# Kernel tuning notes

Hardware: AMD Instinct MI355X
Metric: run time of the kernel (lower is better)

The kernel has to match this reference:

```python
import jax, jax.numpy as jnp
import numpy as np

N, E, B = 25000, 400000, 64      # nodes, edges, graphs per batched graph
NF, EF = 64, 16                  # node / edge input feature sizes
EMB, H = 128, 4                  # GAT embedding size, attention heads
NEG_ATTN, NEG_ACT = 0.2, 0.01    # leaky-relu slopes (attn logits / activations)


def setup_inputs() -> dict:
    keys = iter(jax.random.split(jax.random.key(0), 64))
    def rn(shape, s=0.05):
        return jax.random.normal(next(keys), shape, jnp.float32) * s
    def ri():
        return jax.random.randint(next(keys), (E,), 0, N, jnp.int32)
    # sorted graph ids; construction guarantees every graph is non-empty
    gid = ((jnp.arange(N, dtype=jnp.int32) * B) // N).astype(jnp.int32)
    return dict(
        srcA=ri(), dstA=ri(), gidA=gid,
        nfA=rn((N, NF), 1.0), efA=rn((E, EF), 1.0),
        srcB=ri(), dstB=ri(), gidB=gid,
        nfB=rn((N, NF), 1.0), efB=rn((E, EF), 1.0),
        # stacked params: leading dim 2 = branch (0=A, 1=B)
        p_Wn=rn((2, NF, NF)), p_bn=rn((2, NF)),
        p_We=rn((2, EF, EF)), p_be=rn((2, EF)),
        p_Wc=rn((2, NF + EF, NF + EF)), p_bc=rn((2, NF + EF)),
        p_fc1=rn((2, NF + EF, H * EMB)), p_al1=rn((2, H, EMB)), p_ar1=rn((2, H, EMB)), p_gb1=rn((2, H * EMB)),
        p_Wl1=rn((2, H * EMB, EMB)), p_bl1=rn((2, EMB)),
        p_fc2=rn((2, EMB, H * EMB)), p_al2=rn((2, H, EMB)), p_ar2=rn((2, H, EMB)), p_gb2=rn((2, H * EMB)),
        p_Wl2=rn((2, H * EMB, EMB)), p_bl2=rn((2, EMB)),
        p_ws_w=rn((2, EMB, 1)), p_ws_b=rn((2, 1)),
        p_Wp=rn((2, 2 * EMB, EMB)), p_bp=rn((2, EMB)),
        Wo1=rn((2 * EMB, EMB)), bo1=rn((EMB,)),
        Wo2=rn((EMB, 1)), bo2=rn((1,)),
    )


def _gat(h, src, dst, Wfc, al, ar, bias):
    """DGL GATConv: fc -> per-head attn logits -> edge softmax over dst -> scatter-sum."""
    n = h.shape[0]
    z = (h @ Wfc).reshape(n, al.shape[0], al.shape[1])    # [N,H,D]
    el = jnp.sum(z * al, -1)                              # [N,H]
    er = jnp.sum(z * ar, -1)
    e = jax.nn.leaky_relu(el[src] + er[dst], NEG_ATTN)    # [E,H]
    m = jax.ops.segment_max(e, dst, num_segments=n)
    ex = jnp.exp(e - m[dst])
    a = ex / jax.ops.segment_sum(ex, dst, num_segments=n)[dst]
    rst = jax.ops.segment_sum(a[:, :, None] * z[src], dst, num_segments=n)  # [N,H,D]
    rst = rst + bias.reshape(1, al.shape[0], al.shape[1])
    return jax.nn.leaky_relu(rst, NEG_ACT)                # activation=nn.LeakyReLU()


def _branch(i, src, dst, gid, nf, ef, p):
    n = nf.shape[0]
    # InputInitializer: project nodes/edges, concat src-node feats with edge feats
    hn = nf @ p['p_Wn'][i] + p['p_bn'][i]
    he = ef @ p['p_We'][i] + p['p_be'][i]
    x = jnp.concatenate([hn[src], he], axis=1)            # [E, NF+EF]
    # EdgeGraphConv (in_feats == out_feats -> else-branch): scatter-sum then linear+relu
    x = jax.ops.segment_sum(x, dst, num_segments=n)
    x = jax.nn.relu(x @ p['p_Wc'][i] + p['p_bc'][i])
    # GAT 1 + flatten linear
    x = _gat(x, src, dst, p['p_fc1'][i], p['p_al1'][i], p['p_ar1'][i], p['p_gb1'][i])
    x = x.reshape(n, -1) @ p['p_Wl1'][i] + p['p_bl1'][i]
    # GAT 2 + flatten linear
    x = _gat(x, src, dst, p['p_fc2'][i], p['p_al2'][i], p['p_ar2'][i], p['p_gb2'][i])
    x = x.reshape(n, -1) @ p['p_Wl2'][i] + p['p_bl2'][i]
    # WeightedSumAndMax readout
    w = jax.nn.sigmoid(x @ p['p_ws_w'][i] + p['p_ws_b'][i])
    hs = jax.ops.segment_sum(x * w, gid, num_segments=B)
    hm = jax.ops.segment_max(x, gid, num_segments=B)
    hg = jnp.concatenate([hs, hm], axis=1)                # [B, 2*EMB]
    return hg @ p['p_Wp'][i] + p['p_bp'][i]               # pool_linear


def reference(srcA, dstA, gidA, nfA, efA, srcB, dstB, gidB, nfB, efB,
              p_Wn, p_bn, p_We, p_be, p_Wc, p_bc,
              p_fc1, p_al1, p_ar1, p_gb1, p_Wl1, p_bl1,
              p_fc2, p_al2, p_ar2, p_gb2, p_Wl2, p_bl2,
              p_ws_w, p_ws_b, p_Wp, p_bp, Wo1, bo1, Wo2, bo2):
    p = dict(p_Wn=p_Wn, p_bn=p_bn, p_We=p_We, p_be=p_be, p_Wc=p_Wc, p_bc=p_bc,
             p_fc1=p_fc1, p_al1=p_al1, p_ar1=p_ar1, p_gb1=p_gb1, p_Wl1=p_Wl1, p_bl1=p_bl1,
             p_fc2=p_fc2, p_al2=p_al2, p_ar2=p_ar2, p_gb2=p_gb2, p_Wl2=p_Wl2, p_bl2=p_bl2,
             p_ws_w=p_ws_w, p_ws_b=p_ws_b, p_Wp=p_Wp, p_bp=p_bp)
    x = _branch(0, srcA, dstA, gidA, nfA, efA, p)
    y = _branch(1, srcB, dstB, gidB, nfB, efB, p)
    z = jnp.concatenate([x, y], axis=1)                   # [B, 2*EMB]
    z = jax.nn.leaky_relu(z @ Wo1 + bo1, NEG_ACT)
    return z @ Wo2 + bo2                                  # [B, 1]
```

## Files before the change

### kernel.cpp

```cpp
#include <hip/hip_runtime.h>
#include <hip/hip_bf16.h>
#include <hip/hip_fp16.h>

typedef __hip_bfloat16 bf16;
typedef unsigned short u16;
typedef __attribute__((ext_vector_type(8))) short short8;
typedef __attribute__((ext_vector_type(4))) float floatx4;
typedef _Float16 half8 __attribute__((ext_vector_type(8)));

static constexpr int Nn = 25000;
static constexpr int Ne = 400000;
static constexpr int Bg = 64;

__device__ __forceinline__ float ldf(const void* p, size_t i, bool b16) {
  return b16 ? __bfloat162float(((const bf16*)p)[i]) : ((const float*)p)[i];
}

__global__ void detect_kernel(const u16* a, int n, const u16* b, int m, int* flags) {
  __shared__ int c0, c1;
  if (threadIdx.x == 0) { c0 = 0; c1 = 0; }
  __syncthreads();
  int t = threadIdx.x;
  int l0 = 0, l1 = 0;
  for (int i = t; i < n; i += 256) {
    unsigned e = (a[i] >> 7) & 0xFF;
    if (e >= 140) l0++;
  }
  for (int i = t; i < m; i += 256) {
    unsigned e = (b[i] >> 7) & 0xFF;
    if (e >= 140) l1++;
  }
  atomicAdd(&c0, l0);
  atomicAdd(&c1, l1);
  __syncthreads();
  if (t == 0) {
    flags[0] = (c0 < n / 16) ? 1 : 0;
    flags[1] = (c1 < m / 16) ? 1 : 0;
  }
}

struct TC { const void* W; size_t off; __half* H; int K; int N; int start; };
struct TCAll { TC t[10]; int total; };

__global__ void transconv_all_kernel(TCAll a, const int* __restrict__ pflag) {
  const bool pb = (*pflag != 0);
  int idx = blockIdx.x * 256 + threadIdx.x;
  if (idx >= a.total) return;
  int s = 0;
  while (s + 1 < 10 && idx >= a.t[s + 1].start) s++;
  int li = idx - a.t[s].start;
  int K = a.t[s].K, N = a.t[s].N;
  int k = li / N, n = li - k * N;
  float w = ldf(a.t[s].W, a.t[s].off + li, pb);
  a.t[s].H[(size_t)n * K + k] = __float2half(w);
}

template <int ACT, int OUT>
__global__ __launch_bounds__(256) void mfma_f16_gemm(const __half* __restrict__ A,
                                                     const __half* __restrict__ Bt,
                                                     const void* __restrict__ bias, size_t boff,
                                                     const int* __restrict__ pflag,
                                                     void* __restrict__ C,
                                                     int M, int K, int N) {
  __shared__ short As[128 * 40];
  __shared__ short Bs[128 * 40];
  const int bm = blockIdx.x * 128;
  const int bn = blockIdx.y * 128;
  const int tid = threadIdx.x;
  const int lane = tid & 63;
  const int wave = tid >> 6;
  const int wm = wave >> 1, wn = wave & 1;
  const int lm = lane & 15, quad = lane >> 4;
  const int srow = tid >> 1;
  const int sseg = tid & 1;
  floatx4 acc[4][4] = {};
  for (int k0 = 0; k0 < K; k0 += 32) {
    bool kv = (k0 + sseg * 16) < K;
    {
      int gr = bm + srow;
      short8 a0 = {}, a1 = {};
      if (gr < M && kv) {
        const short8* gp = (const short8*)(A + (size_t)gr * K + k0 + sseg * 16);
        a0 = gp[0];
        a1 = gp[1];
      }
      *(short8*)&As[srow * 40 + sseg * 16] = a0;
      *(short8*)&As[srow * 40 + sseg * 16 + 8] = a1;
    }
    {
      int gc = bn + srow;
      short8 b0 = {}, b1 = {};
      if (gc < N && kv) {
        const short8* gp = (const short8*)(Bt + (size_t)gc * K + k0 + sseg * 16);
        b0 = gp[0];
        b1 = gp[1];
      }
      *(short8*)&Bs[srow * 40 + sseg * 16] = b0;
      *(short8*)&Bs[srow * 40 + sseg * 16 + 8] = b1;
    }
    __syncthreads();
    half8 af[4], bfv[4];
#pragma unroll
    for (int f = 0; f < 4; f++) {
      af[f] = *(const half8*)&As[(wm * 64 + f * 16 + lm) * 40 + quad * 8];
      bfv[f] = *(const half8*)&Bs[(wn * 64 + f * 16 + lm) * 40 + quad * 8];
    }
#pragma unroll
    for (int i = 0; i < 4; i++)
#pragma unroll
      for (int j = 0; j < 4; j++)
        acc[i][j] = __builtin_amdgcn_mfma_f32_16x16x32_f16(af[i], bfv[j], acc[i][j], 0, 0, 0);
    __syncthreads();
  }
  const bool pb = (*pflag != 0);
#pragma unroll
  for (int i = 0; i < 4; i++) {
#pragma unroll
    for (int j = 0; j < 4; j++) {
      int col = bn + wn * 64 + j * 16 + lm;
      if (col >= N) continue;
#pragma unroll
      for (int r = 0; r < 4; r++) {
        int row = bm + wm * 64 + i * 16 + quad * 4 + r;
        if (row >= M) continue;
        float v = acc[i][j][r];
        if (bias) v += ldf(bias, boff + col, pb);
        if (ACT == 1) v = v > 0.f ? v : 0.f;
        if (OUT == 0)
          ((float*)C)[(size_t)row * N + col] = v;
        else
          ((__half*)C)[(size_t)row * N + col] = __float2half(v);
      }
    }
  }
}

__global__ __launch_bounds__(256) void proj_nf_kernel(const void* __restrict__ nfA,
                                                      const void* __restrict__ nfB,
                                                      const int* __restrict__ fflag,
                                                      const void* __restrict__ Wn,
                                                      const void* __restrict__ bn,
                                                      const int* __restrict__ pflag,
                                                      __half* __restrict__ hn, int N) {
  __shared__ float Ws[64 * 65];
  __shared__ float bs[64];
  __shared__ float rowbuf[4][64];
  const bool fb = (*fflag != 0), pb = (*pflag != 0);
  const int b = blockIdx.y;
  const void* nf = b ? nfB : nfA;
  size_t woff = (size_t)b * 64 * 64, boff = (size_t)b * 64;
  int t = threadIdx.x;
  for (int i = t; i < 4096; i += 256) {
    int k = i >> 6, c = i & 63;
    Ws[k * 65 + c] = ldf(Wn, woff + i, pb);
  }
  if (t < 64) bs[t] = ldf(bn, boff + t, pb);
  __syncthreads();
  int wave = t >> 6, lane = t & 63;
  int n = blockIdx.x * 4 + wave;
  if (n >= N) return;
  rowbuf[wave][lane] = ldf(nf, (size_t)n * 64 + lane, fb);
  float acc = bs[lane];
#pragma unroll 8
  for (int k = 0; k < 64; k++) acc += rowbuf[wave][k] * Ws[k * 65 + lane];
  hn[(size_t)b * N * 64 + (size_t)n * 64 + lane] = __float2half(acc);
}

__global__ __launch_bounds__(256) void proj_ef_kernel(const void* __restrict__ efA,
                                                      const void* __restrict__ efB,
                                                      const int* __restrict__ fflag,
                                                      const void* __restrict__ We,
                                                      const void* __restrict__ be,
                                                      const int* __restrict__ pflag,
                                                      __half* __restrict__ he, int E) {
  __shared__ float Ws[16 * 17];
  __shared__ float bs[16];
  __shared__ float efs[16][17];
  const bool fb = (*fflag != 0), pb = (*pflag != 0);
  const int b = blockIdx.y;
  const void* ef = b ? efB : efA;
  size_t woff = (size_t)b * 256, boff = (size_t)b * 16;
  int t = threadIdx.x;
  Ws[(t >> 4) * 17 + (t & 15)] = ldf(We, woff + t, pb);
  if (t < 16) bs[t] = ldf(be, boff + t, pb);
  int el = t >> 4, k = t & 15;
  int e = blockIdx.x * 16 + el;
  float v = 0.f;
  if (e < E) v = ldf(ef, (size_t)e * 16 + k, fb);
  efs[el][k] = v;
  __syncthreads();
  if (e < E) {
    float acc = bs[k];
#pragma unroll
    for (int kk = 0; kk < 16; kk++) acc += efs[el][kk] * Ws[kk * 17 + k];
    he[(size_t)b * E * 16 + (size_t)e * 16 + k] = __float2half(acc);
  }
}

__global__ void count_kernel(const int* __restrict__ dA, const int* __restrict__ dB,
                             int* __restrict__ cnt, int E, int N) {
  int b = blockIdx.y;
  const int* dst = b ? dB : dA;
  int e = blockIdx.x * 256 + threadIdx.x;
  if (e < E) atomicAdd(&cnt[b * N + dst[e]], 1);
}

__global__ void scan1_kernel(const int* __restrict__ cnt, int* __restrict__ incl,
                             int* __restrict__ bsum, int n) {
  __shared__ int buf[256];
  int b = blockIdx.y;
  int t = threadIdx.x;
  int i = blockIdx.x * 256 + t;
  int v = (i < n) ? cnt[b * n + i] : 0;
  buf[t] = v;
  __syncthreads();
  for (int d = 1; d < 256; d <<= 1) {
    int add = (t >= d) ? buf[t - d] : 0;
    __syncthreads();
    buf[t] += add;
    __syncthreads();
  }
  if (i < n) incl[b * n + i] = buf[t];
  if (t == 255) bsum[b * 256 + blockIdx.x] = buf[255];
}

__global__ void scan2_kernel(int* __restrict__ bsum, int nb) {
  __shared__ int buf[256];
  int b = blockIdx.x;
  int t = threadIdx.x;
  int v = (t < nb) ? bsum[b * 256 + t] : 0;
  buf[t] = v;
  __syncthreads();
  for (int d = 1; d < 256; d <<= 1) {
    int add = (t >= d) ? buf[t - d] : 0;
    __syncthreads();
    buf[t] += add;
    __syncthreads();
  }
  if (t < nb) bsum[b * 256 + t] = buf[t] - v;
}

__global__ void scan3_kernel(const int* __restrict__ cnt, const int* __restrict__ incl,
                             const int* __restrict__ bsum, int* __restrict__ offs,
                             int* __restrict__ cursor, int n) {
  int b = blockIdx.y;
  int i = blockIdx.x * 256 + threadIdx.x;
  if (i < n) {
    int e = incl[b * n + i] - cnt[b * n + i] + bsum[b * 256 + blockIdx.x];
    offs[b * (n + 1) + i] = e;
    cursor[b * n + i] = e;
    if (i == n - 1) offs[b * (n + 1) + n] = incl[b * n + i] + bsum[b * 256 + blockIdx.x];
  }
}

__global__ void fill_kernel(const int* __restrict__ dA, const int* __restrict__ dB,
                            int* __restrict__ cursor, int* __restrict__ perm, int E, int N) {
  int b = blockIdx.y;
  const int* dst = b ? dB : dA;
  int e = blockIdx.x * 256 + threadIdx.x;
  if (e < E) {
    int p = atomicAdd(&cursor[b * N + dst[e]], 1);
    perm[(size_t)b * E + p] = e;
  }
}

__global__ __launch_bounds__(64) void sortseg_kernel(const int* __restrict__ off,
                                                     int* __restrict__ perm, int N, int E) {
  __shared__ int loc[64 * 64];
  int b = blockIdx.y;
  const int* offb = off + b * (N + 1);
  int* permb = perm + (size_t)b * E;
  int t = threadIdx.x;
  int n = blockIdx.x * 64 + t;
  if (n >= N) return;
  int e0 = offb[n], e1 = offb[n + 1];
  int d = e1 - e0;
  if (d <= 1) return;
  if (d <= 64) {
    for (int i = 0; i < d; i++) loc[i * 64 + t] = permb[e0 + i];
    for (int i = 1; i < d; i++) {
      int v = loc[i * 64 + t];
      int j = i - 1;
      while (j >= 0 && loc[j * 64 + t] > v) { loc[(j + 1) * 64 + t] = loc[j * 64 + t]; j--; }
      loc[(j + 1) * 64 + t] = v;
    }
    for (int i = 0; i < d; i++) permb[e0 + i] = loc[i * 64 + t];
  } else {
    for (int i = 0; i < d - 1; i++) {
      int mi = i;
      for (int j = i + 1; j < d; j++)
        if (permb[e0 + j] < permb[e0 + mi]) mi = j;
      int tmp = permb[e0 + i];
      permb[e0 + i] = permb[e0 + mi];
      permb[e0 + mi] = tmp;
    }
  }
}

__global__ void srccsr_kernel(const int* __restrict__ sA, const int* __restrict__ sB,
                              const int* __restrict__ perm, int* __restrict__ src_csr, int E) {
  int b = blockIdx.y;
  const int* src = b ? sB : sA;
  int i = blockIdx.x * 256 + threadIdx.x;
  if (i < E) src_csr[(size_t)b * E + i] = src[perm[(size_t)b * E + i]];
}

__global__ __launch_bounds__(128) void edgeconv_kernel(const int* __restrict__ off,
                                                       const int* __restrict__ perm,
                                                       const int* __restrict__ src_csr,
                                                       const __half* __restrict__ hn,
                                                       const __half* __restrict__ he,
                                                       __half* __restrict__ xsum, int N, int E) {
  int b = blockIdx.y;
  const int* offb = off + b * (N + 1);
  const int* permb = perm + (size_t)b * E;
  const int* scb = src_csr + (size_t)b * E;
  const __half* hnb = hn + (size_t)b * N * 64;
  const __half* heb = he + (size_t)b * E * 16;
  int n = blockIdx.x;
  int f = threadIdx.x;
  if (n >= N || f >= 80) return;
  int e0 = offb[n], e1 = offb[n + 1];
  float acc = 0.f;
  if (f < 64) {
    int eg = e0;
    for (; eg + 4 <= e1; eg += 4) {
      int s0 = scb[eg], s1 = scb[eg + 1], s2 = scb[eg + 2], s3 = scb[eg + 3];
      float v0 = __half2float(hnb[(size_t)s0 * 64 + f]);
      float v1 = __half2float(hnb[(size_t)s1 * 64 + f]);
      float v2 = __half2float(hnb[(size_t)s2 * 64 + f]);
      float v3 = __half2float(hnb[(size_t)s3 * 64 + f]);
      acc += v0; acc += v1; acc += v2; acc += v3;
    }
    for (; eg < e1; eg++) acc += __half2float(hnb[(size_t)scb[eg] * 64 + f]);
  } else {
    int c = f - 64;
    for (int eg = e0; eg < e1; eg++) acc += __half2float(heb[(size_t)permb[eg] * 16 + c]);
  }
  xsum[(size_t)b * N * 80 + (size_t)n * 80 + f] = __float2half(acc);
}

__global__ __launch_bounds__(256) void attn_lr_kernel(const __half* __restrict__ z,
                                                      const void* __restrict__ al,
                                                      const void* __restrict__ ar, size_t off,
                                                      const int* __restrict__ pflag,
                                                      float* __restrict__ el,
                                                      float* __restrict__ er, int N) {
  const bool pb = (*pflag != 0);
  int n = (blockIdx.x * blockDim.x + threadIdx.x) >> 6;
  int lane = threadIdx.x & 63;
  if (n >= N) return;
  union { uint4 q; __half s[8]; } u;
  u.q = *(const uint4*)(z + (size_t)n * 512 + lane * 8);
  float sl = 0.f, sr = 0.f;
#pragma unroll
  for (int q = 0; q < 8; q++) {
    int idx = lane * 8 + q;
    float zv = __half2float(u.s[q]);
    sl += zv * ldf(al, off + idx, pb);
    sr += zv * ldf(ar, off + idx, pb);
  }
#pragma unroll
  for (int o = 1; o < 16; o <<= 1) {
    sl += __shfl_xor(sl, o);
    sr += __shfl_xor(sr, o);
  }
  if ((lane & 15) == 0) {
    int h = lane >> 4;
    el[n * 4 + h] = sl;
    er[n * 4 + h] = sr;
  }
}

__global__ void attn_sden_kernel(const int* __restrict__ off, const int* __restrict__ src_csr,
                                 const float* __restrict__ el, const float* __restrict__ er,
                                 float* __restrict__ ecsr, float* __restrict__ sden, int N) {
  int idx = blockIdx.x * 256 + threadIdx.x;
  int n = idx >> 2, h = idx & 3;
  if (n >= N) return;
  int e0 = off[n], e1 = off[n + 1];
  float ern = er[n * 4 + h];
  float s = 0.f;
  for (int eg = e0; eg < e1; eg++) {
    float v = el[src_csr[eg] * 4 + h] + ern;
    v = v > 0.f ? v : 0.2f * v;
    v = fminf(v, 60.f);
    float ev = expf(v);
    ecsr[eg * 4 + h] = ev;
    s += ev;
  }
  sden[n * 4 + h] = s;
}

__global__ __launch_bounds__(256) void gat_gather_kernel(const int* __restrict__ off,
                                                         const int* __restrict__ src_csr,
                                                         const __half* __restrict__ z,
                                                         const float* __restrict__ ecsr,
                                                         const float* __restrict__ sden,
                                                         const void* __restrict__ gb, size_t goff,
                                                         const int* __restrict__ pflag,
                                                         __half* __restrict__ out, int N) {
  const bool pb = (*pflag != 0);
  int n = (blockIdx.x * blockDim.x + threadIdx.x) >> 6;
  int lane = threadIdx.x & 63;
  if (n >= N) return;
  int h = lane >> 4;
  float sd = sden[n * 4 + h];
  float sinv = sd > 0.f ? 1.f / sd : 0.f;
  float acc[8] = {0.f, 0.f, 0.f, 0.f, 0.f, 0.f, 0.f, 0.f};
  int e0 = off[n], e1 = off[n + 1];
  int eg = e0;
  for (; eg + 4 <= e1; eg += 4) {
    int s0 = src_csr[eg], s1 = src_csr[eg + 1], s2 = src_csr[eg + 2], s3 = src_csr[eg + 3];
    float a0 = ecsr[(eg) * 4 + h] * sinv;
    float a1 = ecsr[(eg + 1) * 4 + h] * sinv;
    float a2 = ecsr[(eg + 2) * 4 + h] * sinv;
    float a3 = ecsr[(eg + 3) * 4 + h] * sinv;
    union { uint4 q; __half s[8]; } u0, u1, u2, u3;
    u0.q = *(const uint4*)(z + (size_t)s0 * 512 + lane * 8);
    u1.q = *(const uint4*)(z + (size_t)s1 * 512 + lane * 8);
    u2.q = *(const uint4*)(z + (size_t)s2 * 512 + lane * 8);
    u3.q = *(const uint4*)(z + (size_t)s3 * 512 + lane * 8);
#pragma unroll
    for (int q = 0; q < 8; q++) acc[q] += a0 * __half2float(u0.s[q]);
#pragma unroll
    for (int q = 0; q < 8; q++) acc[q] += a1 * __half2float(u1.s[q]);
#pragma unroll
    for (int q = 0; q < 8; q++) acc[q] += a2 * __half2float(u2.s[q]);
#pragma unroll
    for (int q = 0; q < 8; q++) acc[q] += a3 * __half2float(u3.s[q]);
  }
  for (; eg < e1; eg++) {
    int s0 = src_csr[eg];
    float a0 = ecsr[eg * 4 + h] * sinv;
    union { uint4 q; __half s[8]; } u0;
    u0.q = *(const uint4*)(z + (size_t)s0 * 512 + lane * 8);
#pragma unroll
    for (int q = 0; q < 8; q++) acc[q] += a0 * __half2float(u0.s[q]);
  }
  union { uint4 q; __half s[8]; } w;
#pragma unroll
  for (int q = 0; q < 8; q++) {
    float v = acc[q] + ldf(gb, goff + lane * 8 + q, pb);
    w.s[q] = __float2half(v > 0.f ? v : 0.01f * v);
  }
  *(uint4*)(out + (size_t)n * 512 + lane * 8) = w.q;
}

__global__ __launch_bounds__(256) void wnode_kernel(const float* __restrict__ x,
                                                    const void* __restrict__ wsw, size_t woff,
                                                    const void* __restrict__ wsb, size_t boff,
                                                    const int* __restrict__ pflag,
                                                    float* __restrict__ w, int N) {
  const bool pb = (*pflag != 0);
  int n = (blockIdx.x * blockDim.x + threadIdx.x) >> 6;
  int lane = threadIdx.x & 63;
  if (n >= N) return;
  float s = x[(size_t)n * 128 + lane] * ldf(wsw, woff + lane, pb) +
            x[(size_t)n * 128 + 64 + lane] * ldf(wsw, woff + 64 + lane, pb);
#pragma unroll
  for (int o = 1; o < 64; o <<= 1) s += __shfl_xor(s, o);
  if (lane == 0) {
    float t = s + ldf(wsb, boff, pb);
    t = fmaxf(fminf(t, 60.f), -60.f);
    w[n] = 1.f / (1.f + expf(-t));
  }
}

__device__ __forceinline__ int lower_bound_dev(const int* a, int n, int v) {
  int lo = 0, hi = n;
  while (lo < hi) {
    int mid = (lo + hi) >> 1;
    if (a[mid] < v) lo = mid + 1; else hi = mid;
  }
  return lo;
}

__global__ __launch_bounds__(128) void readout_p1_kernel(const float* __restrict__ x,
                                                         const float* __restrict__ w,
                                                         const int* __restrict__ gid, int N,
                                                         double* __restrict__ psum,
                                                         float* __restrict__ pmax) {
  int g = blockIdx.x >> 4;
  int c = blockIdx.x & 15;
  int d = threadIdx.x;
  __shared__ int ss, se;
  if (d == 0) {
    ss = lower_bound_dev(gid, N, g);
    se = lower_bound_dev(gid, N, g + 1);
  }
  __syncthreads();
  int len = se - ss;
  int a = ss + (int)(((long)len * c) >> 4);
  int b = ss + (int)(((long)len * (c + 1)) >> 4);
  double s = 0.0;
  float m = -1e30f;
  for (int n = a; n < b; n++) {
    float v = x[(size_t)n * 128 + d];
    s += (double)v * (double)w[n];
    m = fmaxf(m, v);
  }
  psum[(size_t)blockIdx.x * 128 + d] = s;
  pmax[(size_t)blockIdx.x * 128 + d] = m;
}

__global__ __launch_bounds__(128) void readout_p2_kernel(const double* __restrict__ psum,
                                                         const float* __restrict__ pmax,
                                                         float* __restrict__ hs,
                                                         float* __restrict__ hm) {
  int g = blockIdx.x, d = threadIdx.x;
  double s = 0.0;
  float m = -1e30f;
#pragma unroll
  for (int c = 0; c < 16; c++) {
    s += psum[(size_t)(g * 16 + c) * 128 + d];
    m = fmaxf(m, pmax[(size_t)(g * 16 + c) * 128 + d]);
  }
  hs[g * 128 + d] = (float)s;
  hm[g * 128 + d] = m;
}

__global__ __launch_bounds__(128) void pool_kernel(const float* __restrict__ hs,
                                                   const float* __restrict__ hm,
                                                   const void* __restrict__ Wp, size_t woff,
                                                   const void* __restrict__ bp, size_t boff,
                                                   const int* __restrict__ pflag,
                                                   float* __restrict__ bout) {
  const bool pb = (*pflag != 0);
  int g = blockIdx.x, j = threadIdx.x;
  __shared__ float hg[256];
  hg[j] = hs[g * 128 + j];
  hg[128 + j] = hm[g * 128 + j];
  __syncthreads();
  double acc = (double)ldf(bp, boff + j, pb);
  for (int k = 0; k < 256; k++) acc += (double)hg[k] * (double)ldf(Wp, woff + (size_t)k * 128 + j, pb);
  bout[g * 128 + j] = (float)acc;
}

__global__ __launch_bounds__(128) void head_kernel(const float* __restrict__ bA,
                                                   const float* __restrict__ bB,
                                                   const void* __restrict__ Wo1,
                                                   const void* __restrict__ bo1,
                                                   const void* __restrict__ Wo2,
                                                   const void* __restrict__ bo2,
                                                   const int* __restrict__ pflag,
                                                   const int* __restrict__ oflag,
                                                   void* __restrict__ out) {
  const bool pb = (*pflag != 0);
  int g = blockIdx.x, j = threadIdx.x;
  __shared__ float zr[256];
  __shared__ double t[128];
  zr[j] = bA[g * 128 + j];
  zr[128 + j] = bB[g * 128 + j];
  __syncthreads();
  double acc = (double)ldf(bo1, j, pb);
  for (int k = 0; k < 256; k++) acc += (double)zr[k] * (double)ldf(Wo1, (size_t)k * 128 + j, pb);
  if (acc < 0.0) acc *= 0.01;
  t[j] = acc * (double)ldf(Wo2, j, pb);
  __syncthreads();
  for (int sdt = 64; sdt > 0; sdt >>= 1) {
    if (j < sdt) t[j] += t[j + sdt];
    __syncthreads();
  }
  if (j == 0) {
    float v = (float)(t[0] + (double)ldf(bo2, 0, pb));
    if (*oflag) ((bf16*)out)[g] = __float2bfloat16(v);
    else ((float*)out)[g] = v;
  }
}

extern "C" void kernel_launch(void* const* d_in, const int* in_sizes, int n_in,
                              void* d_out, int out_size, void* d_ws, size_t ws_size,
                              hipStream_t stream) {
  const int* srcA = (const int*)d_in[0];
  const int* dstA = (const int*)d_in[1];
  const int* gidA = (const int*)d_in[2];
  const void* nfA = d_in[3];
  const void* efA = d_in[4];
  const int* srcB = (const int*)d_in[5];
  const int* dstB = (const int*)d_in[6];
  const int* gidB = (const int*)d_in[7];
  const void* nfB = d_in[8];
  const void* efB = d_in[9];
  const void* p_Wn = d_in[10];
  const void* p_bn = d_in[11];
  const void* p_We = d_in[12];
  const void* p_be = d_in[13];
  const void* p_Wc = d_in[14];
  const void* p_bc = d_in[15];
  const void* p_fc1 = d_in[16];
  const void* p_al1 = d_in[17];
  const void* p_ar1 = d_in[18];
  const void* p_gb1 = d_in[19];
  const void* p_Wl1 = d_in[20];
  const void* p_bl1 = d_in[21];
  const void* p_fc2 = d_in[22];
  const void* p_al2 = d_in[23];
  const void* p_ar2 = d_in[24];
  const void* p_gb2 = d_in[25];
  const void* p_Wl2 = d_in[26];
  const void* p_bl2 = d_in[27];
  const void* p_ws_w = d_in[28];
  const void* p_ws_b = d_in[29];
  const void* p_Wp = d_in[30];
  const void* p_bp = d_in[31];
  const void* Wo1 = d_in[32];
  const void* bo1 = d_in[33];
  const void* Wo2 = d_in[34];
  const void* bo2 = d_in[35];

  char* wp = (char*)d_ws;
  auto alloc = [&](size_t bytes) -> char* {
    char* p = wp;
    wp += (bytes + 255) & ~(size_t)255;
    return p;
  };
  int* flags = (int*)alloc(2 * 4);
  int* cnt = (int*)alloc((size_t)2 * Nn * 4);
  int* incl = (int*)alloc((size_t)2 * Nn * 4);
  int* bsum = (int*)alloc(2 * 256 * 4);
  int* offs = (int*)alloc((size_t)2 * (Nn + 1) * 4);
  int* cursor = (int*)alloc((size_t)2 * Nn * 4);
  int* perm = (int*)alloc((size_t)2 * Ne * 4);
  int* src_csr = (int*)alloc((size_t)2 * Ne * 4);
  float* ecsr = (float*)alloc((size_t)Ne * 4 * 4);
  float* sden = (float*)alloc((size_t)Nn * 4 * 4);
  float* el = (float*)alloc((size_t)Nn * 4 * 4);
  float* er = (float*)alloc((size_t)Nn * 4 * 4);
  float* wn = (float*)alloc((size_t)Nn * 4);
  double* psum = (double*)alloc((size_t)Bg * 16 * 128 * 8);
  float* pmax = (float*)alloc((size_t)Bg * 16 * 128 * 4);
  float* hsb = (float*)alloc((size_t)Bg * 128 * 4);
  float* hmb = (float*)alloc((size_t)Bg * 128 * 4);
  float* bout = (float*)alloc((size_t)2 * Bg * 128 * 4);
  __half* Wct = (__half*)alloc((size_t)2 * 80 * 80 * 2);
  __half* fc1t = (__half*)alloc((size_t)2 * 512 * 80 * 2);
  __half* Wl1t = (__half*)alloc((size_t)2 * 128 * 512 * 2);
  __half* fc2t = (__half*)alloc((size_t)2 * 512 * 128 * 2);
  __half* Wl2t = (__half*)alloc((size_t)2 * 128 * 512 * 2);
  __half* hn = (__half*)alloc((size_t)2 * Nn * 64 * 2);
  __half* he = (__half*)alloc((size_t)2 * Ne * 16 * 2);
  __half* xsum = (__half*)alloc((size_t)2 * Nn * 80 * 2);
  char* zreg = alloc((size_t)Nn * 512 * 2);
  __half* hb = (__half*)alloc((size_t)Nn * 512 * 2);
  __half* xcx1 = (__half*)alloc((size_t)Nn * 128 * 2);
  __half* z = (__half*)zreg;
  float* x2 = (float*)zreg;
  __half* xc = xcx1;
  __half* x1 = xcx1;

  auto cdiv = [](int a, int b) { return (a + b - 1) / b; };

  detect_kernel<<<1, 256, 0, stream>>>((const u16*)nfA, 8192, (const u16*)p_fc1, 8192, flags);
  int* fflag = &flags[0];
  int* pflag = &flags[1];

  {
    TCAll tc;
    int segK[5] = {80, 80, 512, 128, 512};
    int segN[5] = {80, 512, 128, 512, 128};
    const void* segW[5] = {p_Wc, p_fc1, p_Wl1, p_fc2, p_Wl2};
    __half* segH[5] = {Wct, fc1t, Wl1t, fc2t, Wl2t};
    int start = 0, s = 0;
    for (int i = 0; i < 2; i++)
      for (int m = 0; m < 5; m++) {
        int sz = segK[m] * segN[m];
        tc.t[s].W = segW[m];
        tc.t[s].off = (size_t)i * sz;
        tc.t[s].H = segH[m] + (size_t)i * sz;
        tc.t[s].K = segK[m];
        tc.t[s].N = segN[m];
        tc.t[s].start = start;
        start += sz;
        s++;
      }
    tc.total = start;
    transconv_all_kernel<<<cdiv(start, 256), 256, 0, stream>>>(tc, pflag);
  }

  const int nb = cdiv(Nn, 256);

  hipMemsetAsync(cnt, 0, (size_t)2 * Nn * 4, stream);
  count_kernel<<<dim3(cdiv(Ne, 256), 2), 256, 0, stream>>>(dstA, dstB, cnt, Ne, Nn);
  scan1_kernel<<<dim3(nb, 2), 256, 0, stream>>>(cnt, incl, bsum, Nn);
  scan2_kernel<<<2, 256, 0, stream>>>(bsum, nb);
  scan3_kernel<<<dim3(nb, 2), 256, 0, stream>>>(cnt, incl, bsum, offs, cursor, Nn);
  fill_kernel<<<dim3(cdiv(Ne, 256), 2), 256, 0, stream>>>(dstA, dstB, cursor, perm, Ne, Nn);
  sortseg_kernel<<<dim3(cdiv(Nn, 64), 2), 64, 0, stream>>>(offs, perm, Nn, Ne);
  srccsr_kernel<<<dim3(cdiv(Ne, 256), 2), 256, 0, stream>>>(srcA, srcB, perm, src_csr, Ne);
  proj_nf_kernel<<<dim3(cdiv(Nn, 4), 2), 256, 0, stream>>>(
      nfA, nfB, fflag, p_Wn, p_bn, pflag, hn, Nn);
  proj_ef_kernel<<<dim3(cdiv(Ne, 16), 2), 256, 0, stream>>>(
      efA, efB, fflag, p_We, p_be, pflag, he, Ne);
  edgeconv_kernel<<<dim3(Nn, 2), 128, 0, stream>>>(offs, perm, src_csr, hn, he, xsum, Nn, Ne);

  auto run_branch = [&](int i, const int* gid, float* bout_i) {
    const int* offb = offs + i * (Nn + 1);
    const int* scb = src_csr + (size_t)i * Ne;
    mfma_f16_gemm<1, 2><<<dim3(cdiv(Nn, 128), 1), 256, 0, stream>>>(
        xsum + (size_t)i * Nn * 80, Wct + (size_t)i * 80 * 80,
        p_bc, (size_t)i * 80, pflag, xc, Nn, 80, 80);
    mfma_f16_gemm<0, 2><<<dim3(cdiv(Nn, 128), 4), 256, 0, stream>>>(
        xc, fc1t + (size_t)i * 512 * 80, nullptr, 0, pflag, z, Nn, 80, 512);
    attn_lr_kernel<<<cdiv(Nn * 64, 256), 256, 0, stream>>>(
        z, p_al1, p_ar1, (size_t)i * 512, pflag, el, er, Nn);
    attn_sden_kernel<<<cdiv(Nn * 4, 256), 256, 0, stream>>>(offb, scb, el, er, ecsr, sden, Nn);
    gat_gather_kernel<<<cdiv(Nn * 64, 256), 256, 0, stream>>>(
        offb, scb, z, ecsr, sden, p_gb1, (size_t)i * 512, pflag, hb, Nn);
    mfma_f16_gemm<0, 2><<<dim3(cdiv(Nn, 128), 1), 256, 0, stream>>>(
        hb, Wl1t + (size_t)i * 128 * 512, p_bl1, (size_t)i * 128, pflag, x1, Nn, 512, 128);
    mfma_f16_gemm<0, 2><<<dim3(cdiv(Nn, 128), 4), 256, 0, stream>>>(
        x1, fc2t + (size_t)i * 512 * 128, nullptr, 0, pflag, z, Nn, 128, 512);
    attn_lr_kernel<<<cdiv(Nn * 64, 256), 256, 0, stream>>>(
        z, p_al2, p_ar2, (size_t)i * 512, pflag, el, er, Nn);
    attn_sden_kernel<<<cdiv(Nn * 4, 256), 256, 0, stream>>>(offb, scb, el, er, ecsr, sden, Nn);
    gat_gather_kernel<<<cdiv(Nn * 64, 256), 256, 0, stream>>>(
        offb, scb, z, ecsr, sden, p_gb2, (size_t)i * 512, pflag, hb, Nn);
    mfma_f16_gemm<0, 0><<<dim3(cdiv(Nn, 128), 1), 256, 0, stream>>>(
        hb, Wl2t + (size_t)i * 128 * 512, p_bl2, (size_t)i * 128, pflag, x2, Nn, 512, 128);
    wnode_kernel<<<cdiv(Nn * 64, 256), 256, 0, stream>>>(
        x2, p_ws_w, (size_t)i * 128, p_ws_b, (size_t)i, pflag, wn, Nn);
    readout_p1_kernel<<<Bg * 16, 128, 0, stream>>>(x2, wn, gid, Nn, psum, pmax);
    readout_p2_kernel<<<Bg, 128, 0, stream>>>(psum, pmax, hsb, hmb);
    pool_kernel<<<Bg, 128, 0, stream>>>(
        hsb, hmb, p_Wp, (size_t)i * 256 * 128, p_bp, (size_t)i * 128, pflag, bout_i);
  };

  run_branch(0, gidA, bout);
  run_branch(1, gidB, bout + (size_t)Bg * 128);

  head_kernel<<<Bg, 128, 0, stream>>>(bout, bout + (size_t)Bg * 128, Wo1, bo1, Wo2, bo2,
                                      pflag, fflag, d_out);
}
```

Measured before the change: 1.299 ms.

## Batch both branches into single launches and scatter edge features into CSR order

Each per-branch kernel (GEMMs, attention, gather, readout, pool) now takes the branch from a grid dimension, so both branches run in one launch. This halves the launch count and doubles per-launch parallelism for small grids. The edge projection now writes its output directly in CSR order using an inverse permutation computed in srccsr, so edgeconv reads edge features contiguously instead of through perm. Edgeconv is also restructured to one wave per node with a shuffle reduction for the edge part. In exchange, the scratch buffers are doubled and aliased, which uses more memory.

Measured after the change: 1.123 ms. -13.6%, faster.

```diff
diff --git a/kernel.cpp b/kernel.cpp
--- a/kernel.cpp
+++ b/kernel.cpp
@@ -56,12 +56,16 @@
 }
 
 template <int ACT, int OUT>
-__global__ __launch_bounds__(256) void mfma_f16_gemm(const __half* __restrict__ A,
-                                                     const __half* __restrict__ Bt,
-                                                     const void* __restrict__ bias, size_t boff,
+__global__ __launch_bounds__(256) void mfma_f16_gemm(const __half* __restrict__ A, size_t Abs,
+                                                     const __half* __restrict__ Bt, size_t Bbs,
+                                                     const void* __restrict__ bias, size_t bstr,
                                                      const int* __restrict__ pflag,
-                                                     void* __restrict__ C,
+                                                     void* __restrict__ C, size_t Cbs,
                                                      int M, int K, int N) {
+  const int br = blockIdx.z;
+  A += (size_t)br * Abs;
+  Bt += (size_t)br * Bbs;
+  const size_t boff = (size_t)br * bstr;
   __shared__ short As[128 * 40];
   __shared__ short Bs[128 * 40];
   const int bm = blockIdx.x * 128;
@@ -127,9 +131,9 @@
         if (bias) v += ldf(bias, boff + col, pb);
         if (ACT == 1) v = v > 0.f ? v : 0.f;
         if (OUT == 0)
-          ((float*)C)[(size_t)row * N + col] = v;
+          ((float*)C)[(size_t)br * Cbs + (size_t)row * N + col] = v;
         else
-          ((__half*)C)[(size_t)row * N + col] = __float2half(v);
+          ((__half*)C)[(size_t)br * Cbs + (size_t)row * N + col] = __float2half(v);
       }
     }
   }
@@ -172,7 +176,8 @@
                                                       const void* __restrict__ We,
                                                       const void* __restrict__ be,
                                                       const int* __restrict__ pflag,
-                                                      __half* __restrict__ he, int E) {
+                                                      const int* __restrict__ ipos,
+                                                      __half* __restrict__ he_csr, int E) {
   __shared__ float Ws[16 * 17];
   __shared__ float bs[16];
   __shared__ float efs[16][17];
@@ -193,7 +198,8 @@
     float acc = bs[k];
 #pragma unroll
     for (int kk = 0; kk < 16; kk++) acc += efs[el][kk] * Ws[kk * 17 + k];
-    he[(size_t)b * E * 16 + (size_t)e * 16 + k] = __float2half(acc);
+    int pos = ipos[(size_t)b * E + e];
+    he_csr[(size_t)b * E * 16 + (size_t)pos * 16 + k] = __float2half(acc);
   }
 }
 
@@ -298,60 +304,69 @@
 }
 
 __global__ void srccsr_kernel(const int* __restrict__ sA, const int* __restrict__ sB,
-                              const int* __restrict__ perm, int* __restrict__ src_csr, int E) {
+                              const int* __restrict__ perm, int* __restrict__ src_csr,
+                              int* __restrict__ ipos, int E) {
   int b = blockIdx.y;
   const int* src = b ? sB : sA;
   int i = blockIdx.x * 256 + threadIdx.x;
-  if (i < E) src_csr[(size_t)b * E + i] = src[perm[(size_t)b * E + i]];
-}
-
-__global__ __launch_bounds__(128) void edgeconv_kernel(const int* __restrict__ off,
-                                                       const int* __restrict__ perm,
+  if (i < E) {
+    int e = perm[(size_t)b * E + i];
+    src_csr[(size_t)b * E + i] = src[e];
+    ipos[(size_t)b * E + e] = i;
+  }
+}
+
+__global__ __launch_bounds__(256) void edgeconv_kernel(const int* __restrict__ off,
                                                        const int* __restrict__ src_csr,
                                                        const __half* __restrict__ hn,
-                                                       const __half* __restrict__ he,
+                                                       const __half* __restrict__ he_csr,
                                                        __half* __restrict__ xsum, int N, int E) {
   int b = blockIdx.y;
   const int* offb = off + b * (N + 1);
-  const int* permb = perm + (size_t)b * E;
   const int* scb = src_csr + (size_t)b * E;
   const __half* hnb = hn + (size_t)b * N * 64;
-  const __half* heb = he + (size_t)b * E * 16;
-  int n = blockIdx.x;
-  int f = threadIdx.x;
-  if (n >= N || f >= 80) return;
+  const __half* heb = he_csr + (size_t)b * E * 16;
+  int wave = threadIdx.x >> 6, lane = threadIdx.x & 63;
+  int n = blockIdx.x * 4 + wave;
+  if (n >= N) return;
   int e0 = offb[n], e1 = offb[n + 1];
   float acc = 0.f;
-  if (f < 64) {
-    int eg = e0;
-    for (; eg + 4 <= e1; eg += 4) {
-      int s0 = scb[eg], s1 = scb[eg + 1], s2 = scb[eg + 2], s3 = scb[eg + 3];
-      float v0 = __half2float(hnb[(size_t)s0 * 64 + f]);
-      float v1 = __half2float(hnb[(size_t)s1 * 64 + f]);
-      float v2 = __half2float(hnb[(size_t)s2 * 64 + f]);
-      float v3 = __half2float(hnb[(size_t)s3 * 64 + f]);
-      acc += v0; acc += v1; acc += v2; acc += v3;
-    }
-    for (; eg < e1; eg++) acc += __half2float(hnb[(size_t)scb[eg] * 64 + f]);
-  } else {
-    int c = f - 64;
-    for (int eg = e0; eg < e1; eg++) acc += __half2float(heb[(size_t)permb[eg] * 16 + c]);
-  }
-  xsum[(size_t)b * N * 80 + (size_t)n * 80 + f] = __float2half(acc);
+  int eg = e0;
+  for (; eg + 4 <= e1; eg += 4) {
+    int s0 = scb[eg], s1 = scb[eg + 1], s2 = scb[eg + 2], s3 = scb[eg + 3];
+    float v0 = __half2float(hnb[(size_t)s0 * 64 + lane]);
+    float v1 = __half2float(hnb[(size_t)s1 * 64 + lane]);
+    float v2 = __half2float(hnb[(size_t)s2 * 64 + lane]);
+    float v3 = __half2float(hnb[(size_t)s3 * 64 + lane]);
+    acc += v0; acc += v1; acc += v2; acc += v3;
+  }
+  for (; eg < e1; eg++) acc += __half2float(hnb[(size_t)scb[eg] * 64 + lane]);
+  int grp = lane >> 4, f = lane & 15;
+  float hacc = 0.f;
+  for (int e = e0 + grp; e < e1; e += 4) hacc += __half2float(heb[(size_t)e * 16 + f]);
+  hacc += __shfl_xor(hacc, 16);
+  hacc += __shfl_xor(hacc, 32);
+  __half* xr = xsum + (size_t)b * N * 80 + (size_t)n * 80;
+  xr[lane < 64 ? lane : 0] = __float2half(lane < 64 ? acc : acc);
+  xr[lane] = __float2half(acc);
+  if (lane < 16) xr[64 + lane] = __float2half(hacc);
 }
 
 __global__ __launch_bounds__(256) void attn_lr_kernel(const __half* __restrict__ z,
                                                       const void* __restrict__ al,
-                                                      const void* __restrict__ ar, size_t off,
+                                                      const void* __restrict__ ar, size_t astr,
                                                       const int* __restrict__ pflag,
                                                       float* __restrict__ el,
                                                       float* __restrict__ er, int N) {
   const bool pb = (*pflag != 0);
+  const int b = blockIdx.y;
+  const size_t off = (size_t)b * astr;
+  const __half* zb = z + (size_t)b * N * 512;
   int n = (blockIdx.x * blockDim.x + threadIdx.x) >> 6;
   int lane = threadIdx.x & 63;
   if (n >= N) return;
   union { uint4 q; __half s[8]; } u;
-  u.q = *(const uint4*)(z + (size_t)n * 512 + lane * 8);
+  u.q = *(const uint4*)(zb + (size_t)n * 512 + lane * 8);
   float sl = 0.f, sr = 0.f;
 #pragma unroll
   for (int q = 0; q < 8; q++) {
@@ -367,29 +382,34 @@
   }
   if ((lane & 15) == 0) {
     int h = lane >> 4;
-    el[n * 4 + h] = sl;
-    er[n * 4 + h] = sr;
+    el[(size_t)b * N * 4 + n * 4 + h] = sl;
+    er[(size_t)b * N * 4 + n * 4 + h] = sr;
   }
 }
 
 __global__ void attn_sden_kernel(const int* __restrict__ off, const int* __restrict__ src_csr,
                                  const float* __restrict__ el, const float* __restrict__ er,
-                                 float* __restrict__ ecsr, float* __restrict__ sden, int N) {
+                                 float* __restrict__ ecsr, float* __restrict__ sden, int N, int E) {
+  int b = blockIdx.y;
+  const int* offb = off + b * (N + 1);
+  const int* scb = src_csr + (size_t)b * E;
+  const float* elb = el + (size_t)b * N * 4;
+  float* ecb = ecsr + (size_t)b * E * 4;
   int idx = blockIdx.x * 256 + threadIdx.x;
   int n = idx >> 2, h = idx & 3;
   if (n >= N) return;
-  int e0 = off[n], e1 = off[n + 1];
-  float ern = er[n * 4 + h];
+  int e0 = offb[n], e1 = offb[n + 1];
+  float ern = er[(size_t)b * N * 4 + n * 4 + h];
   float s = 0.f;
   for (int eg = e0; eg < e1; eg++) {
-    float v = el[src_csr[eg] * 4 + h] + ern;
+    float v = elb[scb[eg] * 4 + h] + ern;
     v = v > 0.f ? v : 0.2f * v;
     v = fminf(v, 60.f);
     float ev = expf(v);
-    ecsr[eg * 4 + h] = ev;
+    ecb[eg * 4 + h] = ev;
     s += ev;
   }
-  sden[n * 4 + h] = s;
+  sden[(size_t)b * N * 4 + n * 4 + h] = s;
 }
 
 __global__ __launch_bounds__(256) void gat_gather_kernel(const int* __restrict__ off,
@@ -397,30 +417,36 @@
                                                          const __half* __restrict__ z,
                                                          const float* __restrict__ ecsr,
                                                          const float* __restrict__ sden,
-                                                         const void* __restrict__ gb, size_t goff,
+                                                         const void* __restrict__ gb, size_t gstr,
                                                          const int* __restrict__ pflag,
-                                                         __half* __restrict__ out, int N) {
+                                                         __half* __restrict__ out, int N, int E) {
   const bool pb = (*pflag != 0);
+  int b = blockIdx.y;
+  const int* offb = off + b * (N + 1);
+  const int* scb = src_csr + (size_t)b * E;
+  const __half* zb = z + (size_t)b * N * 512;
+  const float* ecb = ecsr + (size_t)b * E * 4;
+  const size_t goff = (size_t)b * gstr;
   int n = (blockIdx.x * blockDim.x + threadIdx.x) >> 6;
   int lane = threadIdx.x & 63;
   if (n >= N) return;
   int h = lane >> 4;
-  float sd = sden[n * 4 + h];
+  float sd = sden[(size_t)b * N * 4 + n * 4 + h];
   float sinv = sd > 0.f ? 1.f / sd : 0.f;
   float acc[8] = {0.f, 0.f, 0.f, 0.f, 0.f, 0.f, 0.f, 0.f};
-  int e0 = off[n], e1 = off[n + 1];
+  int e0 = offb[n], e1 = offb[n + 1];
   int eg = e0;
   for (; eg + 4 <= e1; eg += 4) {
-    int s0 = src_csr[eg], s1 = src_csr[eg + 1], s2 = src_csr[eg + 2], s3 = src_csr[eg + 3];
-    float a0 = ecsr[(eg) * 4 + h] * sinv;
-    float a1 = ecsr[(eg + 1) * 4 + h] * sinv;
-    float a2 = ecsr[(eg + 2) * 4 + h] * sinv;
-    float a3 = ecsr[(eg + 3) * 4 + h] * sinv;
+    int s0 = scb[eg], s1 = scb[eg + 1], s2 = scb[eg + 2], s3 = scb[eg + 3];
+    float a0 = ecb[(eg) * 4 + h] * sinv;
+    float a1 = ecb[(eg + 1) * 4 + h] * sinv;
+    float a2 = ecb[(eg + 2) * 4 + h] * sinv;
+    float a3 = ecb[(eg + 3) * 4 + h] * sinv;
     union { uint4 q; __half s[8]; } u0, u1, u2, u3;
-    u0.q = *(const uint4*)(z + (size_t)s0 * 512 + lane * 8);
-    u1.q = *(const uint4*)(z + (size_t)s1 * 512 + lane * 8);
-    u2.q = *(const uint4*)(z + (size_t)s2 * 512 + lane * 8);
-    u3.q = *(const uint4*)(z + (size_t)s3 * 512 + lane * 8);
+    u0.q = *(const uint4*)(zb + (size_t)s0 * 512 + lane * 8);
+    u1.q = *(const uint4*)(zb + (size_t)s1 * 512 + lane * 8);
+    u2.q = *(const uint4*)(zb + (size_t)s2 * 512 + lane * 8);
+    u3.q = *(const uint4*)(zb + (size_t)s3 * 512 + lane * 8);
 #pragma unroll
     for (int q = 0; q < 8; q++) acc[q] += a0 * __half2float(u0.s[q]);
 #pragma unroll
@@ -431,10 +457,10 @@
     for (int q = 0; q < 8; q++) acc[q] += a3 * __half2float(u3.s[q]);
   }
   for (; eg < e1; eg++) {
-    int s0 = src_csr[eg];
-    float a0 = ecsr[eg * 4 + h] * sinv;
+    int s0 = scb[eg];
+    float a0 = ecb[eg * 4 + h] * sinv;
     union { uint4 q; __half s[8]; } u0;
-    u0.q = *(const uint4*)(z + (size_t)s0 * 512 + lane * 8);
+    u0.q = *(const uint4*)(zb + (size_t)s0 * 512 + lane * 8);
 #pragma unroll
     for (int q = 0; q < 8; q++) acc[q] += a0 * __half2float(u0.s[q]);
   }
@@ -444,26 +470,29 @@
     float v = acc[q] + ldf(gb, goff + lane * 8 + q, pb);
     w.s[q] = __float2half(v > 0.f ? v : 0.01f * v);
   }
-  *(uint4*)(out + (size_t)n * 512 + lane * 8) = w.q;
+  *(uint4*)(out + (size_t)b * N * 512 + (size_t)n * 512 + lane * 8) = w.q;
 }
 
 __global__ __launch_bounds__(256) void wnode_kernel(const float* __restrict__ x,
-                                                    const void* __restrict__ wsw, size_t woff,
-                                                    const void* __restrict__ wsb, size_t boff,
+                                                    const void* __restrict__ wsw,
+                                                    const void* __restrict__ wsb,
                                                     const int* __restrict__ pflag,
                                                     float* __restrict__ w, int N) {
   const bool pb = (*pflag != 0);
+  int b = blockIdx.y;
+  const float* xb = x + (size_t)b * N * 128;
+  size_t woff = (size_t)b * 128, boff = (size_t)b;
   int n = (blockIdx.x * blockDim.x + threadIdx.x) >> 6;
   int lane = threadIdx.x & 63;
   if (n >= N) return;
-  float s = x[(size_t)n * 128 + lane] * ldf(wsw, woff + lane, pb) +
-            x[(size_t)n * 128 + 64 + lane] * ldf(wsw, woff + 64 + lane, pb);
+  float s = xb[(size_t)n * 128 + lane] * ldf(wsw, woff + lane, pb) +
+            xb[(size_t)n * 128 + 64 + lane] * ldf(wsw, woff + 64 + lane, pb);
 #pragma unroll
   for (int o = 1; o < 64; o <<= 1) s += __shfl_xor(s, o);
   if (lane == 0) {
     float t = s + ldf(wsb, boff, pb);
     t = fmaxf(fminf(t, 60.f), -60.f);
-    w[n] = 1.f / (1.f + expf(-t));
+    w[(size_t)b * N + n] = 1.f / (1.f + expf(-t));
   }
 }
 
@@ -478,9 +507,14 @@
 
 __global__ __launch_bounds__(128) void readout_p1_kernel(const float* __restrict__ x,
                                                          const float* __restrict__ w,
-                                                         const int* __restrict__ gid, int N,
+                                                         const int* __restrict__ gidA,
+                                                         const int* __restrict__ gidB, int N,
                                                          double* __restrict__ psum,
                                                          float* __restrict__ pmax) {
+  int b = blockIdx.y;
+  const int* gid = b ? gidB : gidA;
+  const float* xb = x + (size_t)b * N * 128;
+  const float* wb = w + (size_t)b * N;
   int g = blockIdx.x >> 4;
   int c = blockIdx.x & 15;
   int d = threadIdx.x;
@@ -492,49 +526,52 @@
   __syncthreads();
   int len = se - ss;
   int a = ss + (int)(((long)len * c) >> 4);
-  int b = ss + (int)(((long)len * (c + 1)) >> 4);
+  int bb = ss + (int)(((long)len * (c + 1)) >> 4);
   double s = 0.0;
   float m = -1e30f;
-  for (int n = a; n < b; n++) {
-    float v = x[(size_t)n * 128 + d];
-    s += (double)v * (double)w[n];
+  for (int n = a; n < bb; n++) {
+    float v = xb[(size_t)n * 128 + d];
+    s += (double)v * (double)wb[n];
     m = fmaxf(m, v);
   }
-  psum[(size_t)blockIdx.x * 128 + d] = s;
-  pmax[(size_t)blockIdx.x * 128 + d] = m;
+  psum[((size_t)b * Bg * 16 + blockIdx.x) * 128 + d] = s;
+  pmax[((size_t)b * Bg * 16 + blockIdx.x) * 128 + d] = m;
 }
 
 __global__ __launch_bounds__(128) void readout_p2_kernel(const double* __restrict__ psum,
                                                          const float* __restrict__ pmax,
                                                          float* __restrict__ hs,
                                                          float* __restrict__ hm) {
+  int b = blockIdx.y;
   int g = blockIdx.x, d = threadIdx.x;
   double s = 0.0;
   float m = -1e30f;
 #pragma unroll
   for (int c = 0; c < 16; c++) {
-    s += psum[(size_t)(g * 16 + c) * 128 + d];
-    m = fmaxf(m, pmax[(size_t)(g * 16 + c) * 128 + d]);
-  }
-  hs[g * 128 + d] = (float)s;
-  hm[g * 128 + d] = m;
+    s += psum[((size_t)b * Bg * 16 + g * 16 + c) * 128 + d];
+    m = fmaxf(m, pmax[((size_t)b * Bg * 16 + g * 16 + c) * 128 + d]);
+  }
+  hs[(size_t)b * Bg * 128 + g * 128 + d] = (float)s;
+  hm[(size_t)b * Bg * 128 + g * 128 + d] = m;
 }
 
 __global__ __launch_bounds__(128) void pool_kernel(const float* __restrict__ hs,
                                                    const float* __restrict__ hm,
-                                                   const void* __restrict__ Wp, size_t woff,
-                                                   const void* __restrict__ bp, size_t boff,
+                                                   const void* __restrict__ Wp,
+                                                   const void* __restrict__ bp,
                                                    const int* __restrict__ pflag,
                                                    float* __restrict__ bout) {
   const bool pb = (*pflag != 0);
+  int b = blockIdx.y;
+  size_t woff = (size_t)b * 256 * 128, boff = (size_t)b * 128;
   int g = blockIdx.x, j = threadIdx.x;
   __shared__ float hg[256];
-  hg[j] = hs[g * 128 + j];
-  hg[128 + j] = hm[g * 128 + j];
+  hg[j] = hs[(size_t)b * Bg * 128 + g * 128 + j];
+  hg[128 + j] = hm[(size_t)b * Bg * 128 + g * 128 + j];
   __syncthreads();
   double acc = (double)ldf(bp, boff + j, pb);
   for (int k = 0; k < 256; k++) acc += (double)hg[k] * (double)ldf(Wp, woff + (size_t)k * 128 + j, pb);
-  bout[g * 128 + j] = (float)acc;
+  bout[(size_t)b * Bg * 128 + g * 128 + j] = (float)acc;
 }
 
 __global__ __launch_bounds__(128) void head_kernel(const float* __restrict__ bA,
@@ -623,29 +660,31 @@
   int* cursor = (int*)alloc((size_t)2 * Nn * 4);
   int* perm = (int*)alloc((size_t)2 * Ne * 4);
   int* src_csr = (int*)alloc((size_t)2 * Ne * 4);
-  float* ecsr = (float*)alloc((size_t)Ne * 4 * 4);
-  float* sden = (float*)alloc((size_t)Nn * 4 * 4);
-  float* el = (float*)alloc((size_t)Nn * 4 * 4);
-  float* er = (float*)alloc((size_t)Nn * 4 * 4);
-  float* wn = (float*)alloc((size_t)Nn * 4);
-  double* psum = (double*)alloc((size_t)Bg * 16 * 128 * 8);
-  float* pmax = (float*)alloc((size_t)Bg * 16 * 128 * 4);
-  float* hsb = (float*)alloc((size_t)Bg * 128 * 4);
-  float* hmb = (float*)alloc((size_t)Bg * 128 * 4);
+  int* ipos = (int*)alloc((size_t)2 * Ne * 4);
+  float* ecsr = (float*)alloc((size_t)2 * Ne * 4 * 4);
+  float* sden = (float*)alloc((size_t)2 * Nn * 4 * 4);
+  float* el = (float*)alloc((size_t)2 * Nn * 4 * 4);
+  float* er = (float*)alloc((size_t)2 * Nn * 4 * 4);
+  float* wn = (float*)alloc((size_t)2 * Nn * 4);
+  double* psum = (double*)alloc((size_t)2 * Bg * 16 * 128 * 8);
+  float* pmax = (float*)alloc((size_t)2 * Bg * 16 * 128 * 4);
+  float* hsb = (float*)alloc((size_t)2 * Bg * 128 * 4);
+  float* hmb = (float*)alloc((size_t)2 * Bg * 128 * 4);
   float* bout = (float*)alloc((size_t)2 * Bg * 128 * 4);
   __half* Wct = (__half*)alloc((size_t)2 * 80 * 80 * 2);
   __half* fc1t = (__half*)alloc((size_t)2 * 512 * 80 * 2);
   __half* Wl1t = (__half*)alloc((size_t)2 * 128 * 512 * 2);
   __half* fc2t = (__half*)alloc((size_t)2 * 512 * 128 * 2);
   __half* Wl2t = (__half*)alloc((size_t)2 * 128 * 512 * 2);
-  __half* hn = (__half*)alloc((size_t)2 * Nn * 64 * 2);
-  __half* he = (__half*)alloc((size_t)2 * Ne * 16 * 2);
-  __half* xsum = (__half*)alloc((size_t)2 * Nn * 80 * 2);
-  char* zreg = alloc((size_t)Nn * 512 * 2);
-  __half* hb = (__half*)alloc((size_t)Nn * 512 * 2);
-  __half* xcx1 = (__half*)alloc((size_t)Nn * 128 * 2);
-  __half* z = (__half*)zreg;
-  float* x2 = (float*)zreg;
+  char* R = alloc((size_t)2 * Nn * 512 * 2);
+  char* H = alloc((size_t)2 * Nn * 512 * 2);
+  __half* xcx1 = (__half*)alloc((size_t)2 * Nn * 128 * 2);
+  __half* he_csr = (__half*)R;
+  __half* hn = (__half*)(R + (size_t)2 * Ne * 16 * 2);
+  __half* z = (__half*)R;
+  float* x2 = (float*)R;
+  __half* xsum = (__half*)H;
+  __half* hb = (__half*)H;
   __half* xc = xcx1;
   __half* x1 = xcx1;
 
@@ -687,47 +726,47 @@
   scan3_kernel<<<dim3(nb, 2), 256, 0, stream>>>(cnt, incl, bsum, offs, cursor, Nn);
   fill_kernel<<<dim3(cdiv(Ne, 256), 2), 256, 0, stream>>>(dstA, dstB, cursor, perm, Ne, Nn);
   sortseg_kernel<<<dim3(cdiv(Nn, 64), 2), 64, 0, stream>>>(offs, perm, Nn, Ne);
-  srccsr_kernel<<<dim3(cdiv(Ne, 256), 2), 256, 0, stream>>>(srcA, srcB, perm, src_csr, Ne);
+  srccsr_kernel<<<dim3(cdiv(Ne, 256), 2), 256, 0, stream>>>(srcA, srcB, perm, src_csr, ipos, Ne);
   proj_nf_kernel<<<dim3(cdiv(Nn, 4), 2), 256, 0, stream>>>(
       nfA, nfB, fflag, p_Wn, p_bn, pflag, hn, Nn);
   proj_ef_kernel<<<dim3(cdiv(Ne, 16), 2), 256, 0, stream>>>(
-      efA, efB, fflag, p_We, p_be, pflag, he, Ne);
-  edgeconv_kernel<<<dim3(Nn, 2), 128, 0, stream>>>(offs, perm, src_csr, hn, he, xsum, Nn, Ne);
-
-  auto run_branch = [&](int i, const int* gid, float* bout_i) {
-    const int* offb = offs + i * (Nn + 1);
-    const int* scb = src_csr + (size_t)i * Ne;
-    mfma_f16_gemm<1, 2><<<dim3(cdiv(Nn, 128), 1), 256, 0, stream>>>(
-        xsum + (size_t)i * Nn * 80, Wct + (size_t)i * 80 * 80,
-        p_bc, (size_t)i * 80, pflag, xc, Nn, 80, 80);
-    mfma_f16_gemm<0, 2><<<dim3(cdiv(Nn, 128), 4), 256, 0, stream>>>(
-        xc, fc1t + (size_t)i * 512 * 80, nullptr, 0, pflag, z, Nn, 80, 512);
-    attn_lr_kernel<<<cdiv(Nn * 64, 256), 256, 0, stream>>>(
-        z, p_al1, p_ar1, (size_t)i * 512, pflag, el, er, Nn);
-    attn_sden_kernel<<<cdiv(Nn * 4, 256), 256, 0, stream>>>(offb, scb, el, er, ecsr, sden, Nn);
-    gat_gather_kernel<<<cdiv(Nn * 64, 256), 256, 0, stream>>>(
-        offb, scb, z, ecsr, sden, p_gb1, (size_t)i * 512, pflag, hb, Nn);
-    mfma_f16_gemm<0, 2><<<dim3(cdiv(Nn, 128), 1), 256, 0, stream>>>(
-        hb, Wl1t + (size_t)i * 128 * 512, p_bl1, (size_t)i * 128, pflag, x1, Nn, 512, 128);
-    mfma_f16_gemm<0, 2><<<dim3(cdiv(Nn, 128), 4), 256, 0, stream>>>(
-        x1, fc2t + (size_t)i * 512 * 128, nullptr, 0, pflag, z, Nn, 128, 512);
-    attn_lr_kernel<<<cdiv(Nn * 64, 256), 256, 0, stream>>>(
-        z, p_al2, p_ar2, (size_t)i * 512, pflag, el, er, Nn);
-    attn_sden_kernel<<<cdiv(Nn * 4, 256), 256, 0, stream>>>(offb, scb, el, er, ecsr, sden, Nn);
-    gat_gather_kernel<<<cdiv(Nn * 64, 256), 256, 0, stream>>>(
-        offb, scb, z, ecsr, sden, p_gb2, (size_t)i * 512, pflag, hb, Nn);
-    mfma_f16_gemm<0, 0><<<dim3(cdiv(Nn, 128), 1), 256, 0, stream>>>(
-        hb, Wl2t + (size_t)i * 128 * 512, p_bl2, (size_t)i * 128, pflag, x2, Nn, 512, 128);
-    wnode_kernel<<<cdiv(Nn * 64, 256), 256, 0, stream>>>(
-        x2, p_ws_w, (size_t)i * 128, p_ws_b, (size_t)i, pflag, wn, Nn);
-    readout_p1_kernel<<<Bg * 16, 128, 0, stream>>>(x2, wn, gid, Nn, psum, pmax);
-    readout_p2_kernel<<<Bg, 128, 0, stream>>>(psum, pmax, hsb, hmb);
-    pool_kernel<<<Bg, 128, 0, stream>>>(
-        hsb, hmb, p_Wp, (size_t)i * 256 * 128, p_bp, (size_t)i * 128, pflag, bout_i);
-  };
-
-  run_branch(0, gidA, bout);
-  run_branch(1, gidB, bout + (size_t)Bg * 128);
+      efA, efB, fflag, p_We, p_be, pflag, ipos, he_csr, Ne);
+  edgeconv_kernel<<<dim3(cdiv(Nn, 4), 2), 256, 0, stream>>>(
+      offs, src_csr, hn, he_csr, xsum, Nn, Ne);
+
+  const int gm = cdiv(Nn, 128);
+
+  mfma_f16_gemm<1, 2><<<dim3(gm, 1, 2), 256, 0, stream>>>(
+      xsum, (size_t)Nn * 80, Wct, 6400, p_bc, 80, pflag, xc, (size_t)Nn * 80, Nn, 80, 80);
+  mfma_f16_gemm<0, 2><<<dim3(gm, 4, 2), 256, 0, stream>>>(
+      xc, (size_t)Nn * 80, fc1t, (size_t)512 * 80, nullptr, 0, pflag, z, (size_t)Nn * 512,
+      Nn, 80, 512);
+  attn_lr_kernel<<<dim3(cdiv(Nn * 64, 256), 2), 256, 0, stream>>>(
+      z, p_al1, p_ar1, 512, pflag, el, er, Nn);
+  attn_sden_kernel<<<dim3(cdiv(Nn * 4, 256), 2), 256, 0, stream>>>(
+      offs, src_csr, el, er, ecsr, sden, Nn, Ne);
+  gat_gather_kernel<<<dim3(cdiv(Nn * 64, 256), 2), 256, 0, stream>>>(
+      offs, src_csr, z, ecsr, sden, p_gb1, 512, pflag, hb, Nn, Ne);
+  mfma_f16_gemm<0, 2><<<dim3(gm, 1, 2), 256, 0, stream>>>(
+      hb, (size_t)Nn * 512, Wl1t, (size_t)128 * 512, p_bl1, 128, pflag, x1, (size_t)Nn * 128,
+      Nn, 512, 128);
+  mfma_f16_gemm<0, 2><<<dim3(gm, 4, 2), 256, 0, stream>>>(
+      x1, (size_t)Nn * 128, fc2t, (size_t)512 * 128, nullptr, 0, pflag, z, (size_t)Nn * 512,
+      Nn, 128, 512);
+  attn_lr_kernel<<<dim3(cdiv(Nn * 64, 256), 2), 256, 0, stream>>>(
+      z, p_al2, p_ar2, 512, pflag, el, er, Nn);
+  attn_sden_kernel<<<dim3(cdiv(Nn * 4, 256), 2), 256, 0, stream>>>(
+      offs, src_csr, el, er, ecsr, sden, Nn, Ne);
+  gat_gather_kernel<<<dim3(cdiv(Nn * 64, 256), 2), 256, 0, stream>>>(
+      offs, src_csr, z, ecsr, sden, p_gb2, 512, pflag, hb, Nn, Ne);
+  mfma_f16_gemm<0, 0><<<dim3(gm, 1, 2), 256, 0, stream>>>(
+      hb, (size_t)Nn * 512, Wl2t, (size_t)128 * 512, p_bl2, 128, pflag, x2, (size_t)Nn * 128,
+      Nn, 512, 128);
+  wnode_kernel<<<dim3(cdiv(Nn * 64, 256), 2), 256, 0, stream>>>(
+      x2, p_ws_w, p_ws_b, pflag, wn, Nn);
+  readout_p1_kernel<<<dim3(Bg * 16, 2), 128, 0, stream>>>(x2, wn, gidA, gidB, Nn, psum, pmax);
+  readout_p2_kernel<<<dim3(Bg, 2), 128, 0, stream>>>(psum, pmax, hsb, hmb);
+  pool_kernel<<<dim3(Bg, 2), 128, 0, stream>>>(hsb, hmb, p_Wp, p_bp, pflag, bout);
 
   head_kernel<<<Bg, 128, 0, stream>>>(bout, bout + (size_t)Bg * 128, Wo1, bo1, Wo2, bo2,
                                       pflag, fflag, d_out);
```
